# Kernel optimization log

Measured on AMD Instinct MI355X. Metric: run time of the kernel, lower is better.

Reference implementation:

```python
import jax, jax.numpy as jnp
import numpy as np

N_BINS = 64
INPUT_DIM = 8
R = 1.2
BOUND = 10.0
BETA = 1e-06
N = 2097152


def _mesh_and_elmt():
    m = N_BINS / 2
    idx = jnp.arange(N_BINS + 1, dtype=jnp.float32) - m
    x1L = BOUND * (R - 1.0) / (R ** m - 1.0)
    xr = (1.0 - R ** jnp.abs(idx)) / (1.0 - R)
    xr = jnp.where(idx >= 0, x1L * xr, -x1L * xr)
    xr = (xr + BOUND) / (2.0 * BOUND)
    mesh = jnp.concatenate([jnp.zeros((1,), jnp.float32), xr[1:-1], jnp.ones((1,), jnp.float32)])  # [n_bins+1]
    elmt = mesh[1:] - mesh[:-1]  # [n_bins]
    return mesh, elmt


def _pdf_normalize(p, elmt):
    # pdf: [n_bins+1, d]; F_ref: [n_bins, d] cumulative bin integrals
    p0 = jnp.full((1, INPUT_DIM), BETA, jnp.float32)
    ep = jnp.exp(p)
    px = ep * ((elmt[:-1] + elmt[1:]) / 2.0)[:, None]
    scale = (1.0 - (elmt[0] + elmt[-1]) * BETA / 2.0) / jnp.sum(px, 0, keepdims=True)
    px = scale * ep
    pdf = jnp.concatenate([p0, px, p0], 0)
    cell = (pdf[:-1] + pdf[1:]) / 2.0 * elmt[:, None]  # [n_bins, d]
    F_ref = jnp.concatenate([jnp.zeros((1, INPUT_DIM), jnp.float32),
                             jnp.cumsum(cell, 0)[:N_BINS - 1]], 0)
    return pdf, F_ref


def setup_inputs() -> dict:
    key = jax.random.key(0)
    k1, k2 = jax.random.split(key)
    x = jax.random.normal(k1, (N, INPUT_DIM), dtype=jnp.float32)
    logdet = jnp.zeros((N, 1), dtype=jnp.float32)
    p = jax.random.normal(k2, (N_BINS - 1, INPUT_DIM), dtype=jnp.float32)
    return {"x": x, "logdet": logdet, "p": p}


def reference(x, logdet, p):
    mesh, elmt = _mesh_and_elmt()
    pdf, F_ref = _pdf_normalize(p, elmt)

    xs = (x + BOUND) / (2.0 * BOUND)  # [N, d] in [0,1] for covered points
    k = jnp.searchsorted(mesh, xs, side='right') - 1  # [N, d]
    cover = (k >= 0) & (k <= N_BINS - 1)
    k = jnp.clip(k, 0, N_BINS - 1)
    col = jnp.arange(INPUT_DIM)[None, :]

    v1 = pdf[k, col]            # [N, d]
    v2 = pdf[k + 1, col]
    xm = xs - mesh[k]
    h = elmt[k]
    F_pre = F_ref[k, col]

    y = jnp.where(cover, F_pre + xm * xm / 2.0 * (v2 - v1) / h + xm * v1, xs)
    dld = jnp.where(cover, xm * (v2 - v1) / h + v1, 1.0)
    logdet = logdet + jnp.sum(jnp.log(dld), -1, keepdims=True)

    y = y * 2.0 * BOUND - BOUND
    y = jnp.where(y > BOUND, BETA * (y - BOUND) + BOUND, y)
    logdet = logdet + jnp.sum(jnp.log(jnp.where(y > BOUND, BETA, 1.0)), -1, keepdims=True)
    y = jnp.where(y < -BOUND, BETA * (y + BOUND) - BOUND, y)
    logdet = logdet + jnp.sum(jnp.log(jnp.where(y < -BOUND, BETA, 1.0)), -1, keepdims=True)
    return y, logdet
```

## Files before the change

kernel.cpp:

```cpp
#include <hip/hip_runtime.h>
#include <math.h>

#define NDIM   8
#define NBINS  64
#define LOG_BETA   (-13.815510557964274f)
#define LN2F       0.69314718055994531f
#define ALPHA      34.0821892f
#define INV_LOG2R  3.80178401692393f
#define L2R        0.26303440583379378f

typedef float f32x4 __attribute__((ext_vector_type(4)));

__global__ __launch_bounds__(256, 8) void cdfq_fused(const float* __restrict__ x,
                                                     const float* __restrict__ logdet_in,
                                                     const float* __restrict__ p,
                                                     float* __restrict__ y_out,
                                                     float* __restrict__ ld_out,
                                                     int n)
{
    __shared__ float4 stbl[NDIM * NBINS];

    const int t  = threadIdx.x;
    const int T  = gridDim.x * blockDim.x;
    const int i0 = blockIdx.x * blockDim.x + t;
    const int G  = 2 * n;
    const int iters = G / T;
    const float4* xv4 = (const float4*)x;

    float4 X0, X1; float L0, L1;
    if (iters > 0) { X0 = xv4[i0];     L0 = logdet_in[i0 >> 1]; }
    if (iters > 1) { X1 = xv4[i0 + T]; L1 = logdet_in[(i0 + T) >> 1]; }
    __builtin_amdgcn_sched_barrier(0);

    {
        const int lane = t & 63;
        const int w    = t >> 6;
        const float pw32 = exp2f(32.0f * L2R);
        const float inv  = 0.5f / (pw32 - 1.0f);
        auto meshf = [&](float tt) {
            float fidx = tt - 32.0f;
            float pw = exp2f(fabsf(fidx) * L2R);
            float r  = (pw - 1.0f) * inv;
            return 0.5f + ((fidx >= 0.0f) ? r : -r);
        };
        const float m0  = meshf((float)lane);
        const float m1  = meshf((float)(lane + 1));
        const float el  = m1 - m0;
        const float el1 = __shfl_down(el, 1);
        const float e0e63 = 2.0f * (meshf(1.0f) - meshf(0.0f));

#pragma unroll
        for (int dd = 0; dd < 2; ++dd) {
            const int d = 2 * w + dd;
            float ep = 0.0f;
            if (lane < 63) ep = __expf(p[lane * NDIM + d]);
            float s = ep * 0.5f * (el + el1);
#pragma unroll
            for (int off = 32; off; off >>= 1) s += __shfl_xor(s, off);
            const float scale = (1.0f - e0e63 * 5e-7f) / s;
            const float epu = __shfl_up(ep, 1);
            const float pdl = (lane == 0)  ? 1e-6f : scale * epu;
            const float pdn = (lane == 63) ? 1e-6f : scale * ep;
            const float cell = 0.5f * (pdl + pdn) * el;
            float v = cell;
#pragma unroll
            for (int off = 1; off < 64; off <<= 1) {
                float u = __shfl_up(v, off);
                if (lane >= off) v += u;
            }
            stbl[(d << 6) | lane] = make_float4(pdl, (pdn - pdl) / el, v - cell, m0);
        }
    }
    __syncthreads();

    auto body = [&](float4 X, float Lin, int g) {
        const int q     = g >> 1;
        const int dbase = (g & 1) << 2;
        float xd[4] = {X.x, X.y, X.z, X.w};
        float yd[4], dd4[4];
        float extra = 0.0f;

#pragma unroll
        for (int dl = 0; dl < 4; ++dl) {
            float xo = xd[dl];
            float xs = fmaf(xo, 0.05f, 0.5f);
            float gg = __log2f(fmaf(ALPHA, fabsf(xo), 1.0f)) * INV_LOG2R;
            int jf = (int)fminf(gg, 31.0f);
            int k  = (xo >= 0.0f) ? (32 + jf) : (31 - jf);

            float4 tb = stbl[((dbase + dl) << 6) + k];
            float xm  = xs - tb.w;
            bool cov  = (xs >= 0.0f) && (xs < 1.0f);

            float yc = tb.z + xm * fmaf(0.5f * xm, tb.y, tb.x);
            float dv = fmaf(xm, tb.y, tb.x);
            float yy = cov ? yc : xs;
            dd4[dl]  = cov ? dv : 1.0f;

            yy = fmaf(yy, 20.0f, -10.0f);
            if (yy > 10.0f)  { yy = fmaf(1e-6f, yy - 10.0f, 10.0f);  extra += LOG_BETA; }
            if (yy < -10.0f) { yy = fmaf(1e-6f, yy + 10.0f, -10.0f); extra += LOG_BETA; }
            yd[dl] = yy;
        }

        float l2 = __log2f(dd4[0] * dd4[1]) + __log2f(dd4[2] * dd4[3]);
        float contrib = fmaf(l2, LN2F, extra);
        float cross   = __shfl_xor(contrib, 1);

        f32x4 yv = { yd[0], yd[1], yd[2], yd[3] };
        __builtin_nontemporal_store(yv, (f32x4*)y_out + g);
        if ((g & 1) == 0)
            __builtin_nontemporal_store(Lin + contrib + cross, ld_out + q);
    };

    for (int j = 0; j < iters; ++j) {
        float4 Xn; float Ln;
        const bool more = (j + 2 < iters);
        if (more) {
            int gx = i0 + (j + 2) * T;
            Xn = xv4[gx];
            Ln = logdet_in[gx >> 1];
        }
        __builtin_amdgcn_sched_barrier(0);

        body(X0, L0, i0 + j * T);

        X0 = X1; L0 = L1;
        if (more) { X1 = Xn; L1 = Ln; }
    }

    int gr = i0 + iters * T;
    if (gr < G) {
        body(xv4[gr], logdet_in[gr >> 1], gr);
    }
}

extern "C" void kernel_launch(void* const* d_in, const int* in_sizes, int n_in,
                              void* d_out, int out_size, void* d_ws, size_t ws_size,
                              hipStream_t stream) {
    const float* x      = (const float*)d_in[0];
    const float* logdet = (const float*)d_in[1];
    const float* p      = (const float*)d_in[2];

    const int n = in_sizes[1];
    float* y_out  = (float*)d_out;
    float* ld_out = (float*)d_out + (size_t)n * NDIM;

    const int block = 256;
    int grid = 2048;
    if ((long long)grid * block > 2LL * n) grid = (2 * n + block - 1) / block;
    cdfq_fused<<<grid, block, 0, stream>>>(x, logdet, p, y_out, ld_out, n);
}
```

Baseline: 136.3 us.

## Process full rows per thread and preload all four iterations upfront

Each thread now handles one full 8-dim row (two float4 loads) instead of half a row, which removes the cross-lane shuffle for logdet and the duplicated logdet loads. When the grid yields exactly four iterations per thread, all inputs are loaded before the table build, so the global-load latency overlaps the shared-memory setup. The occupancy hint drops from 8 to 6 waves to make room for the extra registers. The costs are lower occupancy and strided 32-byte per-thread accesses, which coalesce less well than the previous contiguous float4 pattern.

Result: slower. 146.4 us (+7.4%).

```diff
diff --git a/kernel.cpp b/kernel.cpp
--- a/kernel.cpp
+++ b/kernel.cpp
@@ -11,7 +11,7 @@
 
 typedef float f32x4 __attribute__((ext_vector_type(4)));
 
-__global__ __launch_bounds__(256, 8) void cdfq_fused(const float* __restrict__ x,
+__global__ __launch_bounds__(256, 6) void cdfq_fused(const float* __restrict__ x,
                                                      const float* __restrict__ logdet_in,
                                                      const float* __restrict__ p,
                                                      float* __restrict__ y_out,
@@ -23,13 +23,20 @@
     const int t  = threadIdx.x;
     const int T  = gridDim.x * blockDim.x;
     const int i0 = blockIdx.x * blockDim.x + t;
-    const int G  = 2 * n;
-    const int iters = G / T;
+    const int iters = n / T;
+    const bool fast = (iters == 4);
     const float4* xv4 = (const float4*)x;
 
-    float4 X0, X1; float L0, L1;
-    if (iters > 0) { X0 = xv4[i0];     L0 = logdet_in[i0 >> 1]; }
-    if (iters > 1) { X1 = xv4[i0 + T]; L1 = logdet_in[(i0 + T) >> 1]; }
+    float4 Xa[4], Xb[4]; float Ld[4];
+    if (fast) {
+#pragma unroll
+        for (int j = 0; j < 4; ++j) {
+            int g = i0 + j * T;
+            Xa[j] = xv4[2 * g];
+            Xb[j] = xv4[2 * g + 1];
+            Ld[j] = logdet_in[g];
+        }
+    }
     __builtin_amdgcn_sched_barrier(0);
 
     {
@@ -73,65 +80,54 @@
     }
     __syncthreads();
 
-    auto body = [&](float4 X, float Lin, int g) {
-        const int q     = g >> 1;
-        const int dbase = (g & 1) << 2;
-        float xd[4] = {X.x, X.y, X.z, X.w};
-        float yd[4], dd4[4];
+    auto body8 = [&](float4 A, float4 B, float Lin, int q) {
+        float xd[8] = {A.x, A.y, A.z, A.w, B.x, B.y, B.z, B.w};
+        float yd[8], dd8[8];
         float extra = 0.0f;
 
 #pragma unroll
-        for (int dl = 0; dl < 4; ++dl) {
-            float xo = xd[dl];
+        for (int d = 0; d < 8; ++d) {
+            float xo = xd[d];
             float xs = fmaf(xo, 0.05f, 0.5f);
             float gg = __log2f(fmaf(ALPHA, fabsf(xo), 1.0f)) * INV_LOG2R;
             int jf = (int)fminf(gg, 31.0f);
             int k  = (xo >= 0.0f) ? (32 + jf) : (31 - jf);
 
-            float4 tb = stbl[((dbase + dl) << 6) + k];
+            float4 tb = stbl[(d << 6) + k];
             float xm  = xs - tb.w;
             bool cov  = (xs >= 0.0f) && (xs < 1.0f);
 
             float yc = tb.z + xm * fmaf(0.5f * xm, tb.y, tb.x);
             float dv = fmaf(xm, tb.y, tb.x);
             float yy = cov ? yc : xs;
-            dd4[dl]  = cov ? dv : 1.0f;
+            dd8[d]   = cov ? dv : 1.0f;
 
             yy = fmaf(yy, 20.0f, -10.0f);
             if (yy > 10.0f)  { yy = fmaf(1e-6f, yy - 10.0f, 10.0f);  extra += LOG_BETA; }
             if (yy < -10.0f) { yy = fmaf(1e-6f, yy + 10.0f, -10.0f); extra += LOG_BETA; }
-            yd[dl] = yy;
+            yd[d] = yy;
         }
 
-        float l2 = __log2f(dd4[0] * dd4[1]) + __log2f(dd4[2] * dd4[3]);
-        float contrib = fmaf(l2, LN2F, extra);
-        float cross   = __shfl_xor(contrib, 1);
+        float q1 = (dd8[0] * dd8[1]) * (dd8[2] * dd8[3]);
+        float q2 = (dd8[4] * dd8[5]) * (dd8[6] * dd8[7]);
+        float contrib = fmaf(__log2f(q1) + __log2f(q2), LN2F, extra);
 
-        f32x4 yv = { yd[0], yd[1], yd[2], yd[3] };
-        __builtin_nontemporal_store(yv, (f32x4*)y_out + g);
-        if ((g & 1) == 0)
-            __builtin_nontemporal_store(Lin + contrib + cross, ld_out + q);
+        f32x4 y1 = { yd[0], yd[1], yd[2], yd[3] };
+        f32x4 y2 = { yd[4], yd[5], yd[6], yd[7] };
+        __builtin_nontemporal_store(y1, (f32x4*)y_out + 2 * q);
+        __builtin_nontemporal_store(y2, (f32x4*)y_out + 2 * q + 1);
+        __builtin_nontemporal_store(Lin + contrib, ld_out + q);
     };
 
-    for (int j = 0; j < iters; ++j) {
-        float4 Xn; float Ln;
-        const bool more = (j + 2 < iters);
-        if (more) {
-            int gx = i0 + (j + 2) * T;
-            Xn = xv4[gx];
-            Ln = logdet_in[gx >> 1];
-        }
-        __builtin_amdgcn_sched_barrier(0);
-
-        body(X0, L0, i0 + j * T);
-
-        X0 = X1; L0 = L1;
-        if (more) { X1 = Xn; L1 = Ln; }
-    }
-
-    int gr = i0 + iters * T;
-    if (gr < G) {
-        body(xv4[gr], logdet_in[gr >> 1], gr);
+    if (fast) {
+#pragma unroll
+        for (int j = 0; j < 4; ++j)
+            body8(Xa[j], Xb[j], Ld[j], i0 + j * T);
+        for (int g = i0 + 4 * T; g < n; g += T)
+            body8(xv4[2 * g], xv4[2 * g + 1], logdet_in[g], g);
+    } else {
+        for (int g = i0; g < n; g += T)
+            body8(xv4[2 * g], xv4[2 * g + 1], logdet_in[g], g);
     }
 }
 
@@ -148,6 +144,6 @@
 
     const int block = 256;
     int grid = 2048;
-    if ((long long)grid * block > 2LL * n) grid = (2 * n + block - 1) / block;
+    if ((long long)grid * block > (long long)n) grid = (n + block - 1) / block;
     cdfq_fused<<<grid, block, 0, stream>>>(x, logdet, p, y_out, ld_out, n);
 }
```

## Issue all eight loads up front in a fully unrolled fast path

Applied to the files above, without the earlier changes.

When each thread has exactly eight items, the kernel issues all eight float4 x loads and logdet loads before the table build, computes them all, then issues all stores together. It lowers the occupancy hint from 8 to 5 waves per SIMD so the extra registers fit. The aim is to hide memory latency through many loads in flight per thread instead of the previous two-deep prefetch. In exchange occupancy drops, and the logdet store no longer uses the nontemporal hint.

After: 143.5 us. 1.05x slower.

```diff
diff --git a/kernel.cpp b/kernel.cpp
--- a/kernel.cpp
+++ b/kernel.cpp
@@ -11,7 +11,7 @@
 
 typedef float f32x4 __attribute__((ext_vector_type(4)));
 
-__global__ __launch_bounds__(256, 8) void cdfq_fused(const float* __restrict__ x,
+__global__ __launch_bounds__(256, 5) void cdfq_fused(const float* __restrict__ x,
                                                      const float* __restrict__ logdet_in,
                                                      const float* __restrict__ p,
                                                      float* __restrict__ y_out,
@@ -25,11 +25,18 @@
     const int i0 = blockIdx.x * blockDim.x + t;
     const int G  = 2 * n;
     const int iters = G / T;
+    const bool fast = (iters == 8) && (iters * T == G);
     const float4* xv4 = (const float4*)x;
 
-    float4 X0, X1; float L0, L1;
-    if (iters > 0) { X0 = xv4[i0];     L0 = logdet_in[i0 >> 1]; }
-    if (iters > 1) { X1 = xv4[i0 + T]; L1 = logdet_in[(i0 + T) >> 1]; }
+    float4 X[8]; float L[8];
+    if (fast) {
+#pragma unroll
+        for (int j = 0; j < 8; ++j) {
+            int g = i0 + j * T;
+            X[j] = xv4[g];
+            L[j] = logdet_in[g >> 1];
+        }
+    }
     __builtin_amdgcn_sched_barrier(0);
 
     {
@@ -73,10 +80,9 @@
     }
     __syncthreads();
 
-    auto body = [&](float4 X, float Lin, int g) {
-        const int q     = g >> 1;
+    auto bodyR = [&](float4 Xv, float Lin, int g, f32x4& Yv, float& LDv) {
         const int dbase = (g & 1) << 2;
-        float xd[4] = {X.x, X.y, X.z, X.w};
+        float xd[4] = {Xv.x, Xv.y, Xv.z, Xv.w};
         float yd[4], dd4[4];
         float extra = 0.0f;
 
@@ -107,31 +113,29 @@
         float contrib = fmaf(l2, LN2F, extra);
         float cross   = __shfl_xor(contrib, 1);
 
-        f32x4 yv = { yd[0], yd[1], yd[2], yd[3] };
-        __builtin_nontemporal_store(yv, (f32x4*)y_out + g);
-        if ((g & 1) == 0)
-            __builtin_nontemporal_store(Lin + contrib + cross, ld_out + q);
+        Yv  = (f32x4){ yd[0], yd[1], yd[2], yd[3] };
+        LDv = Lin + contrib + cross;
     };
 
-    for (int j = 0; j < iters; ++j) {
-        float4 Xn; float Ln;
-        const bool more = (j + 2 < iters);
-        if (more) {
-            int gx = i0 + (j + 2) * T;
-            Xn = xv4[gx];
-            Ln = logdet_in[gx >> 1];
+    if (fast) {
+        f32x4 Y[8]; float LD[8];
+#pragma unroll
+        for (int j = 0; j < 8; ++j)
+            bodyR(X[j], L[j], i0 + j * T, Y[j], LD[j]);
+
+#pragma unroll
+        for (int j = 0; j < 8; ++j) {
+            int g = i0 + j * T;
+            __builtin_nontemporal_store(Y[j], (f32x4*)y_out + g);
+            if ((g & 1) == 0) ld_out[g >> 1] = LD[j];
         }
-        __builtin_amdgcn_sched_barrier(0);
-
-        body(X0, L0, i0 + j * T);
-
-        X0 = X1; L0 = L1;
-        if (more) { X1 = Xn; L1 = Ln; }
-    }
-
-    int gr = i0 + iters * T;
-    if (gr < G) {
-        body(xv4[gr], logdet_in[gr >> 1], gr);
+    } else {
+        for (int g = i0; g < G; g += T) {
+            f32x4 Yv; float LDv;
+            bodyR(xv4[g], logdet_in[g >> 1], g, Yv, LDv);
+            __builtin_nontemporal_store(Yv, (f32x4*)y_out + g);
+            if ((g & 1) == 0) ld_out[g >> 1] = LDv;
+        }
     }
 }
 
```
